# Kernel tuning notes

Measured on AMD Instinct MI355X. Metric: run time of the kernel, lower is better.

## Reference

```python
import jax, jax.numpy as jnp
import numpy as np

TAU = 2.0  # gumbel-softmax temperature (hard=False)


def setup_inputs() -> dict:
    key = jax.random.key(0)
    k = jax.random.split(key, 6)
    b = 128
    names = jax.random.normal(k[0], (b, 256, 30, 32), jnp.float32)
    patterns = jax.random.normal(k[1], (b, 4, 128, 128), jnp.float32)
    attributes = jax.random.normal(k[2], (b, 8, 15, 16), jnp.float32)
    palettes = jax.random.normal(k[3], (b, 8, 12), jnp.float32)
    u1 = jax.random.uniform(k[4], (b, 960, 256), jnp.float32, 1e-6, 1.0 - 1e-6)
    u2 = jax.random.uniform(k[5], (b, 240, 8), jnp.float32, 1e-6, 1.0 - 1e-6)
    gumbel_names = -jnp.log(-jnp.log(u1))
    gumbel_attrs = -jnp.log(-jnp.log(u2))
    return {"names": names, "patterns": patterns, "attributes": attributes,
            "palettes": palettes, "gumbel_names": gumbel_names, "gumbel_attrs": gumbel_attrs}


def reference(names, patterns, attributes, palettes, gumbel_names, gumbel_attrs):
    b = names.shape[0]
    # tile-name logits: (b,256,30,32) -> (b, 960 tiles, 256 names)
    n = names.reshape(b, 256, 30 * 32).transpose(0, 2, 1)
    names_idxs = jax.nn.softmax((n + gumbel_names) / TAU, axis=-1)
    # pattern table: (b,4,128,128) -> 256 tiles of 8x8 pixels x 4 gray levels
    p = patterns.reshape(b, 4, 16, 8, 16, 8).transpose(0, 2, 4, 3, 5, 1)
    p = jax.nn.softmax(p, axis=-1).reshape(b, 256, 8 * 8 * 4)
    # attribute logits: (b,8,15,16) -> (b, 240 blocks, 8 palettes)
    a = attributes.reshape(b, 8, 15 * 16).transpose(0, 2, 1)
    attributes_idxs = jax.nn.softmax((a + gumbel_attrs) / TAU, axis=-1)
    pal = palettes.reshape(b, 8, 4 * 3)
    # soft tile lookup: (b,960,256) @ (b,256,256) -> (b,960,256)
    monochrome = jnp.einsum('btn,bnp->btp', names_idxs, p)
    monochrome = monochrome.reshape(b, 30 * 32, 8 * 8, 4, 1)
    # soft palette lookup: (b,240,8) @ (b,8,12) -> (b,240,12)
    colorization = jnp.einsum('bte,bec->btc', attributes_idxs, pal)
    colorization = colorization.reshape(b, 15, 16, 4, 3)
    # 2x2 attribute-block broadcast to the 30x32 nametable
    colorization = jnp.repeat(jnp.repeat(colorization, 2, axis=1), 2, axis=2)
    colorization = colorization.reshape(b, 30 * 32, 1, 4, 3)
    colorized = (monochrome * colorization).sum(axis=3)  # (b,960,64,3)
    image = colorized.reshape(b, 30, 32, 8, 8, 3).transpose(0, 5, 1, 3, 2, 4)
    image = image.reshape(b, 3, 30 * 8, 32 * 8)
    image = jax.nn.sigmoid(image)
    return image, names_idxs, p, attributes_idxs, pal
```

## Files before the change

kernel.cpp:

```cpp
#include <hip/hip_runtime.h>
#include <hip/hip_bf16.h>
#include <math.h>

#define O_IMG   0
#define O_NAMES 23592960ULL
#define O_P     55050240ULL
#define O_ATTR  63438848ULL
#define O_PAL   63684608ULL

typedef __attribute__((ext_vector_type(8))) short short8v;
typedef __attribute__((ext_vector_type(4))) float f32x4;

static __device__ inline unsigned short f2bf(float x) {
    __hip_bfloat16 h = __float2bfloat16(x);
    return *reinterpret_cast<unsigned short*>(&h);
}

template<bool WRITE_PT>
__global__ __launch_bounds__(256) void k_pattern_t(const float* __restrict__ patterns,
                                                   float* __restrict__ out_p,
                                                   unsigned short* __restrict__ Pt) {
    int idx = blockIdx.x * 256 + threadIdx.x;
    int col = idx & 127;
    int row = (idx >> 7) & 127;
    int b   = idx >> 14;
    const float* base = patterns + (size_t)b * 65536 + row * 128 + col;
    float v0 = base[0];
    float v1 = base[16384];
    float v2 = base[2 * 16384];
    float v3 = base[3 * 16384];
    float m = fmaxf(fmaxf(v0, v1), fmaxf(v2, v3));
    float e0 = expf(v0 - m), e1 = expf(v1 - m), e2 = expf(v2 - m), e3 = expf(v3 - m);
    float inv = 1.0f / (e0 + e1 + e2 + e3);
    float p0 = e0 * inv, p1 = e1 * inv, p2 = e2 * inv, p3 = e3 * inv;
    int ti = row >> 3, pi = row & 7, tj = col >> 3, pj = col & 7;
    int n  = ti * 16 + tj;
    int px = pi * 8 + pj;
    size_t o = ((size_t)(b * 256 + n) * 64 + px) * 4;
    float4 r; r.x = p0; r.y = p1; r.z = p2; r.w = p3;
    *(float4*)(out_p + o) = r;
    if (WRITE_PT) {
        unsigned short* pt = Pt + (size_t)b * 65536 + (size_t)(px * 4) * 256 + n;
        pt[0]   = f2bf(p0);
        pt[256] = f2bf(p1);
        pt[512] = f2bf(p2);
        pt[768] = f2bf(p3);
    }
}

__global__ __launch_bounds__(256) void k_names(const float* __restrict__ names,
                                               const float* __restrict__ gumbel,
                                               float* __restrict__ out) {
    int chunk = blockIdx.x % 60;
    int b     = blockIdx.x / 60;
    int t0 = chunk * 16;
    __shared__ float sN[256 * 17];

    int q = threadIdx.x;
    const float* nb = names + (size_t)b * 245760 + t0;
    {
        int j  = q & 3;
        int n0 = q >> 2;
        #pragma unroll
        for (int pass = 0; pass < 4; pass++) {
            int n = n0 + 64 * pass;
            float4 v = *(const float4*)(nb + (size_t)n * 960 + 4 * j);
            float* dst = sN + n * 17 + 4 * j;
            dst[0] = v.x; dst[1] = v.y; dst[2] = v.z; dst[3] = v.w;
        }
    }
    __syncthreads();

    int lane = q & 63;
    int w    = q >> 6;
    const float* gb = gumbel + ((size_t)b * 960 + t0) * 256;
    float*       ob = out    + ((size_t)b * 960 + t0) * 256;

    #pragma unroll
    for (int tt = 0; tt < 4; tt++) {
        int t = w * 4 + tt;
        float v[4];
        #pragma unroll
        for (int k = 0; k < 4; k++) {
            int n = lane + 64 * k;
            v[k] = (sN[n * 17 + t] + gb[(size_t)t * 256 + n]) * 0.5f;
        }
        float m = fmaxf(fmaxf(v[0], v[1]), fmaxf(v[2], v[3]));
        #pragma unroll
        for (int off = 1; off < 64; off <<= 1) m = fmaxf(m, __shfl_xor(m, off));
        float s = 0.f;
        #pragma unroll
        for (int k = 0; k < 4; k++) { v[k] = expf(v[k] - m); s += v[k]; }
        #pragma unroll
        for (int off = 1; off < 64; off <<= 1) s += __shfl_xor(s, off);
        float inv = 1.0f / s;
        #pragma unroll
        for (int k = 0; k < 4; k++) ob[(size_t)t * 256 + lane + 64 * k] = v[k] * inv;
    }
}

__global__ __launch_bounds__(256) void k_attr(const float* __restrict__ attributes,
                                              const float* __restrict__ gumbel,
                                              const float* __restrict__ palettes,
                                              float* __restrict__ out_attr,
                                              float* __restrict__ out_pal) {
    int idx = blockIdx.x * 256 + threadIdx.x;
    if (idx < 12288) out_pal[idx] = palettes[idx];
    if (idx >= 128 * 240) return;
    int tb = idx % 240;
    int b  = idx / 240;
    float v[8];
    float m = -1e30f;
    #pragma unroll
    for (int e = 0; e < 8; e++) {
        v[e] = (attributes[((size_t)b * 8 + e) * 240 + tb] +
                gumbel[((size_t)b * 240 + tb) * 8 + e]) * 0.5f;
        m = fmaxf(m, v[e]);
    }
    float s = 0.f;
    #pragma unroll
    for (int e = 0; e < 8; e++) { v[e] = expf(v[e] - m); s += v[e]; }
    float inv = 1.0f / s;
    float* o = out_attr + (size_t)idx * 8;
    #pragma unroll
    for (int e = 0; e < 8; e++) o[e] = v[e] * inv;
}

__global__ __launch_bounds__(256, 3) void k_fused(const float* __restrict__ names,
                                                  const float* __restrict__ gumbel,
                                                  const unsigned short* __restrict__ Pt,
                                                  const float* __restrict__ attr,
                                                  const float* __restrict__ pal,
                                                  float* __restrict__ out_names,
                                                  float* __restrict__ img) {
    int j  = blockIdx.x;
    int x  = j & 7;
    int s  = j >> 3;
    int q  = s / 15;
    int rr = s % 15;
    int b  = x + 8 * q;
    int t0 = rr * 64;

    __shared__ __align__(16) char smem[32768];
    __shared__ float sN[256 * 17];
    __shared__ float sCol[192];

    int tid  = threadIdx.x;
    int lane = tid & 63;
    int w    = tid >> 6;
    int lo   = lane & 15;
    int hi   = lane >> 4;

    if (tid < 192) {
        int tbl = tid / 12;
        int gc  = tid % 12;
        int tb  = rr * 16 + tbl;
        const float* at = attr + ((size_t)b * 240 + tb) * 8;
        const float* pl = pal + (size_t)b * 96 + gc;
        float sum = 0.f;
        #pragma unroll
        for (int e = 0; e < 8; e++) sum += at[e] * pl[e * 12];
        sCol[tbl * 12 + gc] = sum;
    }

    const float* nb  = names + (size_t)b * 245760 + t0;
    const float* gb  = gumbel + ((size_t)b * 960 + t0) * 256;
    float*       onb = out_names + ((size_t)b * 960 + t0) * 256;

    for (int c = 0; c < 4; c++) {
        if (c) __syncthreads();
        {
            int jj = tid & 3;
            int n0 = tid >> 2;
            #pragma unroll
            for (int p = 0; p < 4; p++) {
                int n = n0 + 64 * p;
                float4 v = *(const float4*)(nb + (size_t)n * 960 + c * 16 + 4 * jj);
                float* dst = sN + n * 17 + 4 * jj;
                dst[0] = v.x; dst[1] = v.y; dst[2] = v.z; dst[3] = v.w;
            }
        }
        __syncthreads();
        #pragma unroll
        for (int tt = 0; tt < 4; tt++) {
            int trow = w * 4 + tt;
            int tl   = c * 16 + trow;
            float v[4];
            #pragma unroll
            for (int k = 0; k < 4; k++) {
                int n = lane + 64 * k;
                v[k] = (sN[n * 17 + trow] + gb[(size_t)tl * 256 + n]) * 0.5f;
            }
            float m = fmaxf(fmaxf(v[0], v[1]), fmaxf(v[2], v[3]));
            #pragma unroll
            for (int off = 1; off < 64; off <<= 1) m = fmaxf(m, __shfl_xor(m, off));
            float sm = 0.f;
            #pragma unroll
            for (int k = 0; k < 4; k++) { v[k] = expf(v[k] - m); sm += v[k]; }
            #pragma unroll
            for (int off = 1; off < 64; off <<= 1) sm += __shfl_xor(sm, off);
            float inv = 1.0f / sm;
            #pragma unroll
            for (int k = 0; k < 4; k++) {
                int n = lane + 64 * k;
                float p = v[k] * inv;
                onb[(size_t)tl * 256 + n] = p;
                *(unsigned short*)(smem + ((tl * 512 + n * 2) ^ ((tl & 7) << 4))) = f2bf(p);
            }
        }
    }
    __syncthreads();

    f32x4 acc[4][4];
    #pragma unroll
    for (int mi = 0; mi < 4; mi++)
        #pragma unroll
        for (int ni = 0; ni < 4; ni++) acc[mi][ni] = (f32x4){0.f, 0.f, 0.f, 0.f};

    const unsigned short* Ptb = Pt + (size_t)b * 65536 + hi * 8;

    short8v bcur[4], bnxt[4];
    #pragma unroll
    for (int ni = 0; ni < 4; ni++) {
        int f = w * 64 + ni * 16 + lo;
        bcur[ni] = *(const short8v*)(Ptb + (size_t)f * 256);
    }

    #pragma unroll
    for (int k0 = 0; k0 < 256; k0 += 32) {
        if (k0 < 224) {
            #pragma unroll
            for (int ni = 0; ni < 4; ni++) {
                int f = w * 64 + ni * 16 + lo;
                bnxt[ni] = *(const short8v*)(Ptb + (size_t)f * 256 + k0 + 32);
            }
        }
        int ka = (k0 + hi * 8) * 2;
        short8v a0 = *(short8v*)(smem + (((lo      ) * 512 + ka) ^ ((lo & 7) << 4)));
        short8v a1 = *(short8v*)(smem + (((lo + 16) * 512 + ka) ^ ((lo & 7) << 4)));
        short8v a2 = *(short8v*)(smem + (((lo + 32) * 512 + ka) ^ ((lo & 7) << 4)));
        short8v a3 = *(short8v*)(smem + (((lo + 48) * 512 + ka) ^ ((lo & 7) << 4)));
        #pragma unroll
        for (int ni = 0; ni < 4; ni++) {
            acc[0][ni] = __builtin_amdgcn_mfma_f32_16x16x32_bf16(a0, bcur[ni], acc[0][ni], 0, 0, 0);
            acc[1][ni] = __builtin_amdgcn_mfma_f32_16x16x32_bf16(a1, bcur[ni], acc[1][ni], 0, 0, 0);
            acc[2][ni] = __builtin_amdgcn_mfma_f32_16x16x32_bf16(a2, bcur[ni], acc[2][ni], 0, 0, 0);
            acc[3][ni] = __builtin_amdgcn_mfma_f32_16x16x32_bf16(a3, bcur[ni], acc[3][ni], 0, 0, 0);
        }
        if (k0 < 224) {
            #pragma unroll
            for (int ni = 0; ni < 4; ni++) bcur[ni] = bnxt[ni];
        }
    }

    float* sMono = (float*)smem;
    int tf = tid & 63;
    int tm = tid >> 6;
    int pi = tf >> 3, pj = tf & 7;

    #pragma unroll
    for (int mi = 0; mi < 4; mi++) {
        __syncthreads();
        #pragma unroll
        for (int ni = 0; ni < 4; ni++) {
            int colf = w * 64 + ni * 16 + lo;
            #pragma unroll
            for (int rg = 0; rg < 4; rg++)
                sMono[(hi * 4 + rg) * 260 + colf] = acc[mi][ni][rg];
        }
        __syncthreads();
        int r     = rr * 2 + (mi >> 1);
        int cbase = (mi & 1) * 16;
        #pragma unroll
        for (int i = 0; i < 4; i++) {
            int ccl  = tm * 4 + i;
            int ccol = cbase + ccl;
            int tbl  = ccol >> 1;
            float4 mv = *(float4*)&sMono[ccl * 260 + tf * 4];
            #pragma unroll
            for (int c = 0; c < 3; c++) {
                float sv = mv.x * sCol[tbl * 12 + c]
                         + mv.y * sCol[tbl * 12 + 3 + c]
                         + mv.z * sCol[tbl * 12 + 6 + c]
                         + mv.w * sCol[tbl * 12 + 9 + c];
                float y = 1.0f / (1.0f + expf(-sv));
                img[(((size_t)b * 3 + c) * 240 + r * 8 + pi) * 256 + ccol * 8 + pj] = y;
            }
        }
    }
}

__global__ __launch_bounds__(256) void k_image_fp32(const float* __restrict__ A,
                                                    const float* __restrict__ P,
                                                    const float* __restrict__ attr,
                                                    const float* __restrict__ pal,
                                                    float* __restrict__ img) {
    int blk = blockIdx.x;
    int r = blk % 30;
    int b = blk / 30;
    int t0 = r * 32;

    __shared__ float sA[32][33];
    __shared__ float sB[32][256];
    __shared__ float sColF[16][12];

    int tid = threadIdx.x;
    if (tid < 192) {
        int tbl = tid / 12;
        int gc  = tid % 12;
        int tb  = (r >> 1) * 16 + tbl;
        const float* at = attr + ((size_t)b * 240 + tb) * 8;
        const float* pl = pal + (size_t)b * 96 + gc;
        float s = 0.f;
        #pragma unroll
        for (int e = 0; e < 8; e++) s += at[e] * pl[e * 12];
        sColF[tbl][gc] = s;
    }

    float acc[8][4];
    #pragma unroll
    for (int i = 0; i < 8; i++)
        #pragma unroll
        for (int j = 0; j < 4; j++) acc[i][j] = 0.f;

    int tf = tid & 63;
    int tm = tid >> 6;

    const float* Ab = A + ((size_t)b * 960 + t0) * 256;
    const float* Pb = P + (size_t)b * 65536;

    for (int k0 = 0; k0 < 256; k0 += 32) {
        __syncthreads();
        #pragma unroll
        for (int i = 0; i < 4; i++) {
            int li = tid + i * 256;
            int tl = li >> 5, kk = li & 31;
            sA[tl][kk] = Ab[(size_t)tl * 256 + k0 + kk];
        }
        #pragma unroll
        for (int i = 0; i < 8; i++) {
            int li = tid + i * 256;
            int kk = li >> 6, ff = (li & 63) * 4;
            *(float4*)&sB[kk][ff] = *(const float4*)&Pb[(size_t)(k0 + kk) * 256 + ff];
        }
        __syncthreads();
        #pragma unroll
        for (int kk = 0; kk < 32; kk++) {
            float4 bv = *(float4*)&sB[kk][tf * 4];
            #pragma unroll
            for (int i = 0; i < 8; i++) {
                float av = sA[tm * 8 + i][kk];
                acc[i][0] += av * bv.x;
                acc[i][1] += av * bv.y;
                acc[i][2] += av * bv.z;
                acc[i][3] += av * bv.w;
            }
        }
    }

    int pi = tf >> 3, pj = tf & 7;
    #pragma unroll
    for (int i = 0; i < 8; i++) {
        int cc  = tm * 8 + i;
        int tbl = cc >> 1;
        #pragma unroll
        for (int c = 0; c < 3; c++) {
            float s = acc[i][0] * sColF[tbl][c]
                    + acc[i][1] * sColF[tbl][3 + c]
                    + acc[i][2] * sColF[tbl][6 + c]
                    + acc[i][3] * sColF[tbl][9 + c];
            float y = 1.0f / (1.0f + expf(-s));
            img[(((size_t)b * 3 + c) * 240 + r * 8 + pi) * 256 + cc * 8 + pj] = y;
        }
    }
}

extern "C" void kernel_launch(void* const* d_in, const int* in_sizes, int n_in,
                              void* d_out, int out_size, void* d_ws, size_t ws_size,
                              hipStream_t stream) {
    const float* names       = (const float*)d_in[0];
    const float* patterns    = (const float*)d_in[1];
    const float* attributes  = (const float*)d_in[2];
    const float* palettes    = (const float*)d_in[3];
    const float* gumbel_n    = (const float*)d_in[4];
    const float* gumbel_a    = (const float*)d_in[5];
    float* out = (float*)d_out;

    float* out_img   = out + O_IMG;
    float* out_names = out + O_NAMES;
    float* out_p     = out + O_P;
    float* out_attr  = out + O_ATTR;
    float* out_pal   = out + O_PAL;

    const size_t PT_BYTES = 128ULL * 256 * 256 * 2;
    bool use_mfma = (ws_size >= PT_BYTES) && (d_ws != nullptr);

    if (use_mfma) {
        unsigned short* Pt = (unsigned short*)d_ws;
        k_pattern_t<true><<<8192, 256, 0, stream>>>(patterns, out_p, Pt);
        k_attr<<<120, 256, 0, stream>>>(attributes, gumbel_a, palettes, out_attr, out_pal);
        k_fused<<<1920, 256, 0, stream>>>(names, gumbel_n, Pt, out_attr, palettes,
                                          out_names, out_img);
    } else {
        k_pattern_t<false><<<8192, 256, 0, stream>>>(patterns, out_p, nullptr);
        k_names<<<128 * 60, 256, 0, stream>>>(names, gumbel_n, out_names);
        k_attr<<<120, 256, 0, stream>>>(attributes, gumbel_a, palettes, out_attr, out_pal);
        k_image_fp32<<<128 * 30, 256, 0, stream>>>(out_names, out_p, out_attr, palettes, out_img);
    }
}
```

Measured before the change: 168.8 us.

## Tile pattern softmax through LDS, halve fused-kernel tile, use fast exp

The pattern kernel is rewritten so each block stages one pixel row of all 256 tiles in shared memory. It then writes out_p and the transposed bf16 Pt table with coalesced vector stores instead of strided 2-byte scatters. The fused names/matmul/image kernel now handles 32 tiles per block instead of 64, doubling the grid, shrinking LDS and accumulators, and raising the occupancy hint to 4. expf is replaced by __expf throughout. The smaller tile means each block rereads the full Pt B-matrix for half the work, so B traffic per output doubles.

```diff
diff --git a/kernel.cpp b/kernel.cpp
--- a/kernel.cpp
+++ b/kernel.cpp
@@ -17,34 +17,64 @@
 }
 
 template<bool WRITE_PT>
-__global__ __launch_bounds__(256) void k_pattern_t(const float* __restrict__ patterns,
-                                                   float* __restrict__ out_p,
-                                                   unsigned short* __restrict__ Pt) {
-    int idx = blockIdx.x * 256 + threadIdx.x;
-    int col = idx & 127;
-    int row = (idx >> 7) & 127;
-    int b   = idx >> 14;
-    const float* base = patterns + (size_t)b * 65536 + row * 128 + col;
-    float v0 = base[0];
-    float v1 = base[16384];
-    float v2 = base[2 * 16384];
-    float v3 = base[3 * 16384];
-    float m = fmaxf(fmaxf(v0, v1), fmaxf(v2, v3));
-    float e0 = expf(v0 - m), e1 = expf(v1 - m), e2 = expf(v2 - m), e3 = expf(v3 - m);
-    float inv = 1.0f / (e0 + e1 + e2 + e3);
-    float p0 = e0 * inv, p1 = e1 * inv, p2 = e2 * inv, p3 = e3 * inv;
-    int ti = row >> 3, pi = row & 7, tj = col >> 3, pj = col & 7;
-    int n  = ti * 16 + tj;
-    int px = pi * 8 + pj;
-    size_t o = ((size_t)(b * 256 + n) * 64 + px) * 4;
-    float4 r; r.x = p0; r.y = p1; r.z = p2; r.w = p3;
-    *(float4*)(out_p + o) = r;
+__global__ __launch_bounds__(256) void k_pattern2(const float* __restrict__ patterns,
+                                                  float* __restrict__ out_p,
+                                                  unsigned short* __restrict__ Pt) {
+    int bp = blockIdx.x;
+    int b  = bp >> 3;
+    int pi = bp & 7;
+
+    __shared__ float sP[4 * 16 * 136];
+    __shared__ unsigned short sR[32 * 264];
+
+    int tid = threadIdx.x;
+
+    #pragma unroll
+    for (int p = 0; p < 8; p++) {
+        int li   = p * 256 + tid;
+        int col4 = li & 31;
+        int ti   = (li >> 5) & 15;
+        int g    = li >> 9;
+        float4 v = *(const float4*)(patterns + (size_t)b * 65536 + g * 16384 +
+                                    (ti * 8 + pi) * 128 + col4 * 4);
+        *(float4*)&sP[(g * 16 + ti) * 136 + col4 * 4] = v;
+    }
+    __syncthreads();
+
+    int pj = tid & 7;
+    int nb = tid >> 3;
+    #pragma unroll
+    for (int i = 0; i < 8; i++) {
+        int n  = nb * 8 + i;
+        int ti = n >> 4, tj = n & 15;
+        int base = ti * 136 + tj * 8 + pj;
+        float v0 = sP[              base];
+        float v1 = sP[16 * 136   + base];
+        float v2 = sP[32 * 136   + base];
+        float v3 = sP[48 * 136   + base];
+        float m  = fmaxf(fmaxf(v0, v1), fmaxf(v2, v3));
+        float e0 = __expf(v0 - m), e1 = __expf(v1 - m), e2 = __expf(v2 - m), e3 = __expf(v3 - m);
+        float inv = 1.0f / (e0 + e1 + e2 + e3);
+        float p0 = e0 * inv, p1 = e1 * inv, p2 = e2 * inv, p3 = e3 * inv;
+        float4 r; r.x = p0; r.y = p1; r.z = p2; r.w = p3;
+        *(float4*)(out_p + (size_t)(b * 256 + n) * 256 + pi * 32 + pj * 4) = r;
+        if (WRITE_PT) {
+            sR[(pj * 4 + 0) * 264 + n] = f2bf(p0);
+            sR[(pj * 4 + 1) * 264 + n] = f2bf(p1);
+            sR[(pj * 4 + 2) * 264 + n] = f2bf(p2);
+            sR[(pj * 4 + 3) * 264 + n] = f2bf(p3);
+        }
+    }
     if (WRITE_PT) {
-        unsigned short* pt = Pt + (size_t)b * 65536 + (size_t)(px * 4) * 256 + n;
-        pt[0]   = f2bf(p0);
-        pt[256] = f2bf(p1);
-        pt[512] = f2bf(p2);
-        pt[768] = f2bf(p3);
+        __syncthreads();
+        int n4  = tid & 63;
+        int fl0 = tid >> 6;
+        #pragma unroll
+        for (int k = 0; k < 8; k++) {
+            int fl = fl0 * 8 + k;
+            short4 rv = *(short4*)&sR[fl * 264 + n4 * 4];
+            *(short4*)(Pt + (size_t)b * 65536 + (size_t)(pi * 32 + fl) * 256 + n4 * 4) = rv;
+        }
     }
 }
 
@@ -119,14 +149,14 @@
     }
     float s = 0.f;
     #pragma unroll
-    for (int e = 0; e < 8; e++) { v[e] = expf(v[e] - m); s += v[e]; }
+    for (int e = 0; e < 8; e++) { v[e] = __expf(v[e] - m); s += v[e]; }
     float inv = 1.0f / s;
     float* o = out_attr + (size_t)idx * 8;
     #pragma unroll
     for (int e = 0; e < 8; e++) o[e] = v[e] * inv;
 }
 
-__global__ __launch_bounds__(256, 3) void k_fused(const float* __restrict__ names,
+__global__ __launch_bounds__(256, 4) void k_fused(const float* __restrict__ names,
                                                   const float* __restrict__ gumbel,
                                                   const unsigned short* __restrict__ Pt,
                                                   const float* __restrict__ attr,
@@ -136,12 +166,12 @@
     int j  = blockIdx.x;
     int x  = j & 7;
     int s  = j >> 3;
-    int q  = s / 15;
-    int rr = s % 15;
+    int q  = s / 30;
+    int rr = s % 30;
     int b  = x + 8 * q;
-    int t0 = rr * 64;
-
-    __shared__ __align__(16) char smem[32768];
+    int t0 = rr * 32;
+
+    __shared__ __align__(16) char smem[16896];
     __shared__ float sN[256 * 17];
     __shared__ float sCol[192];
 
@@ -154,7 +184,7 @@
     if (tid < 192) {
         int tbl = tid / 12;
         int gc  = tid % 12;
-        int tb  = rr * 16 + tbl;
+        int tb  = (rr >> 1) * 16 + tbl;
         const float* at = attr + ((size_t)b * 240 + tb) * 8;
         const float* pl = pal + (size_t)b * 96 + gc;
         float sum = 0.f;
@@ -167,7 +197,7 @@
     const float* gb  = gumbel + ((size_t)b * 960 + t0) * 256;
     float*       onb = out_names + ((size_t)b * 960 + t0) * 256;
 
-    for (int c = 0; c < 4; c++) {
+    for (int c = 0; c < 2; c++) {
         if (c) __syncthreads();
         {
             int jj = tid & 3;
@@ -196,7 +226,7 @@
             for (int off = 1; off < 64; off <<= 1) m = fmaxf(m, __shfl_xor(m, off));
             float sm = 0.f;
             #pragma unroll
-            for (int k = 0; k < 4; k++) { v[k] = expf(v[k] - m); sm += v[k]; }
+            for (int k = 0; k < 4; k++) { v[k] = __expf(v[k] - m); sm += v[k]; }
             #pragma unroll
             for (int off = 1; off < 64; off <<= 1) sm += __shfl_xor(sm, off);
             float inv = 1.0f / sm;
@@ -211,9 +241,9 @@
     }
     __syncthreads();
 
-    f32x4 acc[4][4];
-    #pragma unroll
-    for (int mi = 0; mi < 4; mi++)
+    f32x4 acc[2][4];
+    #pragma unroll
+    for (int mi = 0; mi < 2; mi++)
         #pragma unroll
         for (int ni = 0; ni < 4; ni++) acc[mi][ni] = (f32x4){0.f, 0.f, 0.f, 0.f};
 
@@ -238,14 +268,10 @@
         int ka = (k0 + hi * 8) * 2;
         short8v a0 = *(short8v*)(smem + (((lo      ) * 512 + ka) ^ ((lo & 7) << 4)));
         short8v a1 = *(short8v*)(smem + (((lo + 16) * 512 + ka) ^ ((lo & 7) << 4)));
-        short8v a2 = *(short8v*)(smem + (((lo + 32) * 512 + ka) ^ ((lo & 7) << 4)));
-        short8v a3 = *(short8v*)(smem + (((lo + 48) * 512 + ka) ^ ((lo & 7) << 4)));
         #pragma unroll
         for (int ni = 0; ni < 4; ni++) {
             acc[0][ni] = __builtin_amdgcn_mfma_f32_16x16x32_bf16(a0, bcur[ni], acc[0][ni], 0, 0, 0);
             acc[1][ni] = __builtin_amdgcn_mfma_f32_16x16x32_bf16(a1, bcur[ni], acc[1][ni], 0, 0, 0);
-            acc[2][ni] = __builtin_amdgcn_mfma_f32_16x16x32_bf16(a2, bcur[ni], acc[2][ni], 0, 0, 0);
-            acc[3][ni] = __builtin_amdgcn_mfma_f32_16x16x32_bf16(a3, bcur[ni], acc[3][ni], 0, 0, 0);
         }
         if (k0 < 224) {
             #pragma unroll
@@ -259,7 +285,7 @@
     int pi = tf >> 3, pj = tf & 7;
 
     #pragma unroll
-    for (int mi = 0; mi < 4; mi++) {
+    for (int mi = 0; mi < 2; mi++) {
         __syncthreads();
         #pragma unroll
         for (int ni = 0; ni < 4; ni++) {
@@ -269,8 +295,7 @@
                 sMono[(hi * 4 + rg) * 260 + colf] = acc[mi][ni][rg];
         }
         __syncthreads();
-        int r     = rr * 2 + (mi >> 1);
-        int cbase = (mi & 1) * 16;
+        int cbase = mi * 16;
         #pragma unroll
         for (int i = 0; i < 4; i++) {
             int ccl  = tm * 4 + i;
@@ -283,8 +308,8 @@
                          + mv.y * sCol[tbl * 12 + 3 + c]
                          + mv.z * sCol[tbl * 12 + 6 + c]
                          + mv.w * sCol[tbl * 12 + 9 + c];
-                float y = 1.0f / (1.0f + expf(-sv));
-                img[(((size_t)b * 3 + c) * 240 + r * 8 + pi) * 256 + ccol * 8 + pj] = y;
+                float y = 1.0f / (1.0f + __expf(-sv));
+                img[(((size_t)b * 3 + c) * 240 + rr * 8 + pi) * 256 + ccol * 8 + pj] = y;
             }
         }
     }
@@ -397,12 +422,12 @@
 
     if (use_mfma) {
         unsigned short* Pt = (unsigned short*)d_ws;
-        k_pattern_t<true><<<8192, 256, 0, stream>>>(patterns, out_p, Pt);
+        k_pattern2<true><<<1024, 256, 0, stream>>>(patterns, out_p, Pt);
         k_attr<<<120, 256, 0, stream>>>(attributes, gumbel_a, palettes, out_attr, out_pal);
-        k_fused<<<1920, 256, 0, stream>>>(names, gumbel_n, Pt, out_attr, palettes,
+        k_fused<<<3840, 256, 0, stream>>>(names, gumbel_n, Pt, out_attr, palettes,
                                           out_names, out_img);
     } else {
-        k_pattern_t<false><<<8192, 256, 0, stream>>>(patterns, out_p, nullptr);
+        k_pattern2<false><<<1024, 256, 0, stream>>>(patterns, out_p, nullptr);
         k_names<<<128 * 60, 256, 0, stream>>>(names, gumbel_n, out_names);
         k_attr<<<120, 256, 0, stream>>>(attributes, gumbel_a, palettes, out_attr, out_pal);
         k_image_fp32<<<128 * 30, 256, 0, stream>>>(out_names, out_p, out_attr, palettes, out_img);
```

Measured after the change: 169.9 us. Within noise of the previous version (+0.6%).
